# Performance work log

Measured on AMD Instinct MI355X. Metric: run time of the kernel, lower is better.

## Reference

```python
import jax, jax.numpy as jnp
import numpy as np

N, E, E_LG, H, KGE, NUM_GRAPHS, N_ITER = 100000, 500000, 1000000, 128, 128, 1024, 2
EPS = 1e-5

def _prelu(x, a):
    return jnp.where(x >= 0, x, a * x)

def _seg_mean(vals, idx, num):
    s = jax.ops.segment_sum(vals, idx, num_segments=num)
    c = jax.ops.segment_sum(jnp.ones((vals.shape[0],), vals.dtype), idx, num_segments=num)
    return s / jnp.maximum(c, 1.0)[:, None]

def setup_inputs() -> dict:
    key = jax.random.key(0)
    ks = jax.random.split(key, 16)
    sc = 1.0 / np.sqrt(H)
    inp = {
        "x": jax.random.normal(ks[0], (N, H), jnp.float32),
        "edge_attr": jax.random.normal(ks[1], (E, H), jnp.float32),
        "edge_index": jax.random.randint(ks[2], (2, E), 0, N),
        "batch": jnp.sort(jax.random.randint(ks[3], (N,), 0, NUM_GRAPHS)),
        "line_graph_edge_index": jax.random.randint(ks[4], (2, E_LG), 0, E),
        # edge_update_net: Linear + PReLU + BatchNorm1d (eval mode)
        "W1": jax.random.normal(ks[5], (H, H), jnp.float32) * sc,
        "b1": jnp.zeros((H,), jnp.float32),
        "a1": jnp.full((1,), 0.25, jnp.float32),
        "bn_gamma": jnp.ones((H,), jnp.float32),
        "bn_beta": jnp.zeros((H,), jnp.float32),
        "bn_mean": jnp.zeros((H,), jnp.float32),
        "bn_var": jnp.ones((H,), jnp.float32),
        # GRU (single layer, single step)
        "w_ih": jax.random.normal(ks[6], (3 * H, H), jnp.float32) * sc,
        "w_hh": jax.random.normal(ks[7], (3 * H, H), jnp.float32) * sc,
        "b_ih": jnp.zeros((3 * H,), jnp.float32),
        "b_hh": jnp.zeros((3 * H,), jnp.float32),
        # DynamicAttention net
        "Wa1": jax.random.normal(ks[8], (H // 2, H), jnp.float32) * sc,
        "ba1": jnp.zeros((H // 2,), jnp.float32),
        "a2": jnp.full((1,), 0.25, jnp.float32),
        "Wa2": jax.random.normal(ks[9], (1, H // 2), jnp.float32) * (1.0 / np.sqrt(H // 2)),
        "ba2": jnp.zeros((1,), jnp.float32),
        # readout
        "Wr": jax.random.normal(ks[10], (KGE, H), jnp.float32) * sc,
        "br": jnp.zeros((KGE,), jnp.float32),
    }
    return inp

def reference(x, edge_attr, W1, b1, a1, bn_gamma, bn_beta, bn_mean, bn_var,
              w_ih, w_hh, b_ih, b_hh, Wa1, ba1, a2, Wa2, ba2, Wr, br,
              edge_index, batch, line_graph_edge_index):
    src, dst = edge_index[0], edge_index[1]
    l_src, l_dst = line_graph_edge_index[0], line_graph_edge_index[1]
    h = x  # GRU hidden state [N, H]
    for _ in range(N_ITER):
        # edge-to-edge message passing (node_to_edge_proj is Identity here)
        fused = edge_attr + (x[src] + x[dst]) * 0.5  # [E, H]
        agg = _seg_mean(fused[l_src], l_dst, E)      # scatter-mean over line graph
        upd = _prelu(agg @ W1.T + b1, a1)
        upd = (upd - bn_mean) * jax.lax.rsqrt(bn_var + EPS) * bn_gamma + bn_beta
        fused = fused + upd
        node_updates = _seg_mean(fused, dst, N)      # [N, H]
        # single GRU step
        gi = node_updates @ w_ih.T + b_ih
        gh = h @ w_hh.T + b_hh
        gi_r, gi_z, gi_n = jnp.split(gi, 3, axis=-1)
        gh_r, gh_z, gh_n = jnp.split(gh, 3, axis=-1)
        r = jax.nn.sigmoid(gi_r + gh_r)
        z = jax.nn.sigmoid(gi_z + gh_z)
        n = jnp.tanh(gi_n + r * gh_n)
        h = (1.0 - z) * n + z * h
        x = h
    # dynamic attention: per-graph scalar gate
    graph_repr = _seg_mean(x, batch, NUM_GRAPHS)     # [G, H]
    attn = jax.nn.sigmoid(_prelu(graph_repr @ Wa1.T + ba1, a2) @ Wa2.T + ba2)  # [G, 1]
    attended = x * attn[batch]
    graph_emb = jax.ops.segment_sum(attended, batch, num_segments=NUM_GRAPHS)
    graph_emb = graph_emb @ Wr.T + br
    return (x, graph_emb)
```

## Files before the change

kernel.cpp:

```cpp
#include <hip/hip_runtime.h>
#include <stdint.h>

#define H 128
#define G_NUM 1024
#define BN_EPS 1e-5f
#define IDXCAP 512

typedef unsigned int uint;
typedef unsigned short ushort;
typedef unsigned char uchar;
typedef __attribute__((ext_vector_type(8))) __bf16 bf16x8;
typedef __attribute__((ext_vector_type(8))) ushort ushort8;
typedef __attribute__((ext_vector_type(4))) float f32x4;
typedef __attribute__((ext_vector_type(2))) float f32x2;

__device__ __forceinline__ float b2f(ushort u){ return __uint_as_float(((uint)u) << 16); }
__device__ __forceinline__ ushort f2b(float f){
    uint u = __float_as_uint(f);
    u += 0x7FFFu + ((u >> 16) & 1u);
    return (ushort)(u >> 16);
}
__device__ __forceinline__ float ldf(const void* p, size_t i, int bf){
    return bf ? b2f(((const ushort*)p)[i]) : ((const float*)p)[i];
}
__device__ __forceinline__ int swz(int r, int byte_in_row){
    return (r * 256 + byte_in_row) ^ ((r & 7) << 4);
}

#define GBODY(SRC, sA, sB) do{ \
    uint4 wA_ = *(const uint4*)((SRC) + (size_t)(sA) * H + ch16 * 8); \
    uint4 wB_ = *(const uint4*)((SRC) + (size_t)(sB) * H + ch16 * 8); \
    uint wa_[4] = {wA_.x, wA_.y, wA_.z, wA_.w}; \
    uint wb_[4] = {wB_.x, wB_.y, wB_.z, wB_.w}; \
    _Pragma("unroll") \
    for (int k2 = 0; k2 < 4; k2++){ \
        f32x2 va_, vb_; \
        va_.x = __uint_as_float(wa_[k2] << 16); va_.y = __uint_as_float(wa_[k2] & 0xFFFF0000u); \
        vb_.x = __uint_as_float(wb_[k2] << 16); vb_.y = __uint_as_float(wb_[k2] & 0xFFFF0000u); \
        accA[k2] += va_; accB[k2] += vb_; \
    } }while(0)

__global__ void k_setup_small(const uint* __restrict__ gamma_bits,
                              const void* b1, const void* a1, const void* gam, const void* bet,
                              const void* mean, const void* var, const void* bih, const void* bhh,
                              float* __restrict__ ep, float* __restrict__ bi, float* __restrict__ bh,
                              int* __restrict__ flag, ushort* __restrict__ fz1, ushort* __restrict__ fz2,
                              size_t zoff, int* __restrict__ off_cat, int nk_idx, int sent_val){
    __shared__ int bfs;
    int t = threadIdx.x;
    if (t == 0){
        int f = (gamma_bits[0] == 0x3F803F80u) ? 1 : 0;
        *flag = f; bfs = f;
        off_cat[nk_idx] = sent_val;
    }
    __syncthreads();
    int bf = bfs;
    bi[t] = ldf(bih, t, bf);
    bh[t] = ldf(bhh, t, bf);
    if (t < 128){
        ep[t]       = ldf(b1, t, bf);
        ep[128 + t] = rsqrtf(ldf(var, t, bf) + BN_EPS) * ldf(gam, t, bf);
        ep[256 + t] = ldf(mean, t, bf);
        ep[384 + t] = ldf(bet, t, bf);
        fz1[zoff + t] = 0; fz2[zoff + t] = 0;
    }
    if (t == 0) ep[512] = ldf(a1, 0, bf);
}

__global__ __launch_bounds__(256) void k_count2(const int* __restrict__ lgi, const int* __restrict__ ei,
                                                int* __restrict__ cnt, int ELG, int E){
    int t = blockIdx.x * 256 + threadIdx.x;
    if (t < ELG) atomicAdd(&cnt[lgi[ELG + t]], 1);
    else { int t2 = t - ELG; if (t2 < E) atomicAdd(&cnt[E + ei[E + t2]], 1); }
}
__global__ __launch_bounds__(256) void k_scan_reduce(const int* __restrict__ cnt, int* __restrict__ bsum, int n){
    int base = blockIdx.x * 1024;
    int s = 0;
    for (int i = threadIdx.x; i < 1024; i += 256){ int idx = base + i; s += (idx < n) ? cnt[idx] : 0; }
    __shared__ int r[256];
    r[threadIdx.x] = s; __syncthreads();
    for (int o = 128; o > 0; o >>= 1){ if (threadIdx.x < o) r[threadIdx.x] += r[threadIdx.x + o]; __syncthreads(); }
    if (threadIdx.x == 0) bsum[blockIdx.x] = r[0];
}
__global__ __launch_bounds__(256) void k_scan_mid(int* __restrict__ bsum, int nb){
    __shared__ int ts[256];
    int tid = threadIdx.x;
    int loc[4]; int s = 0;
    #pragma unroll
    for (int j = 0; j < 4; j++){
        int idx = tid * 4 + j;
        loc[j] = s;
        s += (idx < nb) ? bsum[idx] : 0;
    }
    ts[tid] = s; __syncthreads();
    for (int o = 1; o < 256; o <<= 1){
        int v = (tid >= o) ? ts[tid - o] : 0;
        __syncthreads();
        ts[tid] += v;
        __syncthreads();
    }
    int texcl = ts[tid] - s;
    #pragma unroll
    for (int j = 0; j < 4; j++){
        int idx = tid * 4 + j;
        if (idx < nb) bsum[idx] = texcl + loc[j];
    }
}
__global__ __launch_bounds__(256) void k_scan_final(const int* __restrict__ cnt, const int* __restrict__ bsum,
                                                    int* __restrict__ off, int n){
    __shared__ int ts[256];
    int base = blockIdx.x * 1024;
    int tid = threadIdx.x;
    int loc[4]; int s = 0;
    #pragma unroll
    for (int j = 0; j < 4; j++){
        int idx = base + tid * 4 + j;
        loc[j] = s;
        s += (idx < n) ? cnt[idx] : 0;
    }
    ts[tid] = s; __syncthreads();
    for (int o = 1; o < 256; o <<= 1){
        int v = (tid >= o) ? ts[tid - o] : 0;
        __syncthreads();
        ts[tid] += v;
        __syncthreads();
    }
    int texcl = ts[tid] - s + bsum[blockIdx.x];
    #pragma unroll
    for (int j = 0; j < 4; j++){
        int idx = base + tid * 4 + j;
        if (idx < n) off[idx] = texcl + loc[j];
    }
}
__global__ __launch_bounds__(256) void k_fill2(const int* __restrict__ lgi, const int* __restrict__ ei,
                                               const int* __restrict__ off, int* __restrict__ cur,
                                               int* __restrict__ list, int ELG, int E){
    int t = blockIdx.x * 256 + threadIdx.x;
    if (t < ELG){
        int k = lgi[ELG + t];
        int pos = atomicAdd(&cur[k], 1);
        list[off[k] + pos] = lgi[t];
    } else {
        int t2 = t - ELG;
        if (t2 < E){
            int k = E + ei[E + t2];
            int pos = atomicAdd(&cur[k], 1);
            list[off[k] + pos] = t2;
        }
    }
}
__global__ __launch_bounds__(256) void k_sortperm(const int* __restrict__ off, uchar* __restrict__ perm, int NK){
    int t = blockIdx.x * 256 + threadIdx.x;
    int wave = t >> 6;
    int l = t & 63;
    int l5 = l & 31;
    int r0 = wave * 32;
    if (r0 >= NK) return;
    int r = r0 + l5;
    int deg = off[r + 1] - off[r];
    int key = (deg << 5) | l5;
    #pragma unroll
    for (int k = 2; k <= 32; k <<= 1){
        #pragma unroll
        for (int j = k >> 1; j > 0; j >>= 1){
            int other = __shfl_xor(key, j);
            bool dir = ((l5 & k) == 0);
            bool lower = ((l5 & j) == 0);
            int mn = min(key, other), mx = max(key, other);
            key = (dir == lower) ? mn : mx;
        }
    }
    if (l < 32) perm[r0 + l5] = (uchar)(key & 31);
}
__global__ __launch_bounds__(256) void k_cvt_bf(const void* __restrict__ in, ushort* __restrict__ out,
                                                int n, const int* __restrict__ flag){
    int t = blockIdx.x * 256 + threadIdx.x;
    if (t >= n) return;
    if (*flag) out[t] = ((const ushort*)in)[t];
    else       out[t] = f2b(((const float*)in)[t]);
}
__global__ __launch_bounds__(256) void k_wcvt(const void* __restrict__ W1, const void* __restrict__ wih,
                                              const void* __restrict__ whh, const void* __restrict__ Wr,
                                              ushort* __restrict__ W1bf, ushort* __restrict__ wihbf,
                                              ushort* __restrict__ whhbf, float* __restrict__ WrT,
                                              const int* __restrict__ flag){
    int t = blockIdx.x * 256 + threadIdx.x;
    int bf = *flag;
    if (t < 16384) W1bf[t] = bf ? ((const ushort*)W1)[t] : f2b(((const float*)W1)[t]);
    else if (t < 65536){ int i = t - 16384; wihbf[i] = bf ? ((const ushort*)wih)[i] : f2b(((const float*)wih)[i]); }
    else if (t < 114688){ int i = t - 65536; whhbf[i] = bf ? ((const ushort*)whh)[i] : f2b(((const float*)whh)[i]); }
    else if (t < 131072){ int i = t - 114688; int r = i >> 7, c = i & 127; WrT[c * 128 + r] = ldf(Wr, i, bf); }
}

__global__ __launch_bounds__(256) void k_fused(const void* __restrict__ ea, const ushort* __restrict__ hb,
                                               const int* __restrict__ ei, ushort* __restrict__ fused,
                                               int E, const int* __restrict__ flag){
    int t = blockIdx.x * 256 + threadIdx.x;
    if (t >= E * 16) return;
    int bf = *flag;
    int e = t >> 4, ch = (t & 15) * 8;
    int s = ei[e], d = ei[E + e];
    ushort8 hs = *(const ushort8*)(hb + (size_t)s * H + ch);
    ushort8 hd = *(const ushort8*)(hb + (size_t)d * H + ch);
    size_t base = (size_t)e * H + ch;
    float av[8];
    if (bf){
        ushort8 a = *(const ushort8*)((const ushort*)ea + base);
        #pragma unroll
        for (int j = 0; j < 8; j++) av[j] = b2f(a[j]);
    } else {
        float4 a0 = *(const float4*)((const float*)ea + base);
        float4 a1 = *(const float4*)((const float*)ea + base + 4);
        av[0] = a0.x; av[1] = a0.y; av[2] = a0.z; av[3] = a0.w;
        av[4] = a1.x; av[5] = a1.y; av[6] = a1.z; av[7] = a1.w;
    }
    ushort8 o;
    #pragma unroll
    for (int j = 0; j < 8; j++) o[j] = f2b(av[j] + 0.5f * (b2f(hs[j]) + b2f(hd[j])));
    *(ushort8*)(fused + base) = o;
}

__global__ __launch_bounds__(256) void k_agg_gemm(const ushort* __restrict__ fused,
                                                  const int* __restrict__ off_cat, const int* __restrict__ list,
                                                  const uchar* __restrict__ perm,
                                                  const ushort* __restrict__ W1bf, const float* __restrict__ ep,
                                                  ushort* __restrict__ fused2, int E, int LMAX){
    __shared__ __attribute__((aligned(16))) char As[32 * 256];
    __shared__ int idxL[IDXCAP];
    __shared__ int offL[33];
    int tid = threadIdx.x, wid = tid >> 6, lane = tid & 63;
    int r0 = blockIdx.x * 32;
    if (tid < 33) offL[tid] = off_cat[r0 + tid];
    __syncthreads();
    int seg_s = offL[0], seglen = offL[32] - seg_s;
    bool staged = (seglen <= IDXCAP);
    if (staged){ for (int j = tid; j < seglen; j += 256) idxL[j] = list[seg_s + j]; }
    __syncthreads();
    int l16 = lane >> 4, ch16 = lane & 15;
    int rA = wid * 8 + l16, rB = rA + 4;
    int plA = perm[r0 + rA], plB = perm[r0 + rB];
    int baseA = offL[plA], degA = offL[plA + 1] - baseA;
    int baseB = offL[plB], degB = offL[plB + 1] - baseB;
    int dm = max(degA, degB);
    #pragma unroll
    for (int o = 32; o > 0; o >>= 1) dm = max(dm, __shfl_xor(dm, o));
    f32x2 accA[4] = {}, accB[4] = {};
    if (staged){
        int relA = baseA - seg_s, relB = baseB - seg_s;
        #pragma unroll 2
        for (int i = 0; i < dm; i++){
            int liA = min(relA + i, seglen - 1);
            int liB = min(relB + i, seglen - 1);
            int sA = idxL[liA];
            int sB = idxL[liB];
            sA = (i < degA) ? sA : E;
            sB = (i < degB) ? sB : E;
            GBODY(fused, sA, sB);
        }
    } else {
        #pragma unroll 2
        for (int i = 0; i < dm; i++){
            int liA = baseA + i; liA = (liA < LMAX) ? liA : (LMAX - 1);
            int liB = baseB + i; liB = (liB < LMAX) ? liB : (LMAX - 1);
            int sA = list[liA];
            int sB = list[liB];
            sA = (i < degA) ? sA : E;
            sB = (i < degB) ? sB : E;
            GBODY(fused, sA, sB);
        }
    }
    float invA = 1.f / fmaxf((float)degA, 1.f);
    float invB = 1.f / fmaxf((float)degB, 1.f);
    ushort8 oA, oB;
    #pragma unroll
    for (int k2 = 0; k2 < 4; k2++){
        oA[2 * k2] = f2b(accA[k2].x * invA); oA[2 * k2 + 1] = f2b(accA[k2].y * invA);
        oB[2 * k2] = f2b(accB[k2].x * invB); oB[2 * k2 + 1] = f2b(accB[k2].y * invB);
    }
    *(ushort8*)(As + swz(plA, ch16 * 16)) = oA;
    *(ushort8*)(As + swz(plB, ch16 * 16)) = oB;
    __syncthreads();
    int lrow = lane & 15, lhi = lane >> 4;
    f32x4 acc[2][2] = {};
    #pragma unroll
    for (int ks = 0; ks < 4; ks++){
        bf16x8 afr[2];
        #pragma unroll
        for (int rt = 0; rt < 2; rt++)
            afr[rt] = *(const bf16x8*)(As + swz(rt * 16 + lrow, ks * 64 + lhi * 16));
        #pragma unroll
        for (int cc = 0; cc < 2; cc++){
            int c = (2 * wid + cc) * 16 + lrow;
            bf16x8 bfr = *(const bf16x8*)(W1bf + (size_t)c * H + ks * 32 + lhi * 8);
            #pragma unroll
            for (int rt = 0; rt < 2; rt++)
                acc[cc][rt] = __builtin_amdgcn_mfma_f32_16x16x32_bf16(afr[rt], bfr, acc[cc][rt], 0, 0, 0);
        }
    }
    __syncthreads();
    float aa = ep[512];
    #pragma unroll
    for (int cc = 0; cc < 2; cc++){
        int c = (2 * wid + cc) * 16 + lrow;
        float bb = ep[c], sc = ep[128 + c], mb = ep[256 + c], be = ep[384 + c];
        #pragma unroll
        for (int rt = 0; rt < 2; rt++)
            #pragma unroll
            for (int rg = 0; rg < 4; rg++){
                int r = rt * 16 + lhi * 4 + rg;
                float u = acc[cc][rt][rg] + bb;
                u = (u >= 0.f) ? u : aa * u;
                u = (u - mb) * sc + be;
                *(ushort*)(As + swz(r, c * 2)) = f2b(u);
            }
    }
    __syncthreads();
    #pragma unroll
    for (int q = 0; q < 2; q++){
        int r = (q == 0) ? rA : rB;
        size_t gbase = (size_t)(r0 + r) * H + ch16 * 8;
        ushort8 f = *(const ushort8*)(fused + gbase);
        ushort8 u = *(const ushort8*)(As + swz(r, ch16 * 16));
        ushort8 o;
        #pragma unroll
        for (int j = 0; j < 8; j++) o[j] = f2b(b2f(f[j]) + b2f(u[j]));
        *(ushort8*)(fused2 + gbase) = o;
    }
}

__global__ __launch_bounds__(256) void k_gru(const ushort* __restrict__ fused2,
                                             const int* __restrict__ off_cat, const int* __restrict__ list,
                                             const uchar* __restrict__ perm,
                                             ushort* __restrict__ hb,
                                             const ushort* __restrict__ wihbf, const ushort* __restrict__ whhbf,
                                             const float* __restrict__ bi, const float* __restrict__ bh,
                                             int N, int EZ, int LMAX){
    __shared__ __attribute__((aligned(16))) char NUs[32 * 256];
    __shared__ __attribute__((aligned(16))) char HHs[32 * 256];
    __shared__ int idxL[IDXCAP];
    __shared__ int offL[33];
    int tid = threadIdx.x, wid = tid >> 6, lane = tid & 63;
    int r0 = blockIdx.x * 32;
    if (tid < 33) offL[tid] = off_cat[r0 + tid];
    int l16 = lane >> 4, ch16 = lane & 15;
    int rA = wid * 8 + l16, rB = rA + 4;
    *(ushort8*)(HHs + swz(rA, ch16 * 16)) = *(const ushort8*)(hb + (size_t)(r0 + rA) * H + ch16 * 8);
    *(ushort8*)(HHs + swz(rB, ch16 * 16)) = *(const ushort8*)(hb + (size_t)(r0 + rB) * H + ch16 * 8);
    __syncthreads();
    int seg_s = offL[0], seglen = offL[32] - seg_s;
    bool staged = (seglen <= IDXCAP);
    if (staged){ for (int j = tid; j < seglen; j += 256) idxL[j] = list[seg_s + j]; }
    __syncthreads();
    int plA = perm[r0 + rA], plB = perm[r0 + rB];
    int baseA = offL[plA], degA = offL[plA + 1] - baseA;
    int baseB = offL[plB], degB = offL[plB + 1] - baseB;
    int dm = max(degA, degB);
    #pragma unroll
    for (int o = 32; o > 0; o >>= 1) dm = max(dm, __shfl_xor(dm, o));
    f32x2 accA[4] = {}, accB[4] = {};
    if (staged){
        int relA = baseA - seg_s, relB = baseB - seg_s;
        #pragma unroll 2
        for (int i = 0; i < dm; i++){
            int liA = min(relA + i, seglen - 1);
            int liB = min(relB + i, seglen - 1);
            int sA = idxL[liA];
            int sB = idxL[liB];
            sA = (i < degA) ? sA : EZ;
            sB = (i < degB) ? sB : EZ;
            GBODY(fused2, sA, sB);
        }
    } else {
        #pragma unroll 2
        for (int i = 0; i < dm; i++){
            int liA = baseA + i; liA = (liA < LMAX) ? liA : (LMAX - 1);
            int liB = baseB + i; liB = (liB < LMAX) ? liB : (LMAX - 1);
            int sA = list[liA];
            int sB = list[liB];
            sA = (i < degA) ? sA : EZ;
            sB = (i < degB) ? sB : EZ;
            GBODY(fused2, sA, sB);
        }
    }
    float invA = 1.f / fmaxf((float)degA, 1.f);
    float invB = 1.f / fmaxf((float)degB, 1.f);
    ushort8 oA, oB;
    #pragma unroll
    for (int k2 = 0; k2 < 4; k2++){
        oA[2 * k2] = f2b(accA[k2].x * invA); oA[2 * k2 + 1] = f2b(accA[k2].y * invA);
        oB[2 * k2] = f2b(accB[k2].x * invB); oB[2 * k2 + 1] = f2b(accB[k2].y * invB);
    }
    *(ushort8*)(NUs + swz(plA, ch16 * 16)) = oA;
    *(ushort8*)(NUs + swz(plB, ch16 * 16)) = oB;
    __syncthreads();
    int lrow = lane & 15, lhi = lane >> 4;
    ushort hnew[2][2][4];
    #pragma unroll 1
    for (int b = 0; b < 2; b++){
        f32x4 aI[3][2] = {}, aH[3][2] = {};
        #pragma unroll
        for (int ks = 0; ks < 4; ks++){
            bf16x8 fN[2], fH[2];
            #pragma unroll
            for (int rt = 0; rt < 2; rt++){
                int addr = swz(rt * 16 + lrow, ks * 64 + lhi * 16);
                fN[rt] = *(const bf16x8*)(NUs + addr);
                fH[rt] = *(const bf16x8*)(HHs + addr);
            }
            #pragma unroll
            for (int g = 0; g < 3; g++){
                int c = g * 128 + (wid + 4 * b) * 16 + lrow;
                bf16x8 bI = *(const bf16x8*)(wihbf + (size_t)c * H + ks * 32 + lhi * 8);
                bf16x8 bH = *(const bf16x8*)(whhbf + (size_t)c * H + ks * 32 + lhi * 8);
                #pragma unroll
                for (int rt = 0; rt < 2; rt++){
                    aI[g][rt] = __builtin_amdgcn_mfma_f32_16x16x32_bf16(fN[rt], bI, aI[g][rt], 0, 0, 0);
                    aH[g][rt] = __builtin_amdgcn_mfma_f32_16x16x32_bf16(fH[rt], bH, aH[g][rt], 0, 0, 0);
                }
            }
        }
        int c = (wid + 4 * b) * 16 + lrow;
        float bir = bi[c], biz = bi[128 + c], bin = bi[256 + c];
        float bhr = bh[c], bhz = bh[128 + c], bhn = bh[256 + c];
        #pragma unroll
        for (int rt = 0; rt < 2; rt++)
            #pragma unroll
            for (int rg = 0; rg < 4; rg++){
                int r = rt * 16 + lhi * 4 + rg;
                float gr = aI[0][rt][rg] + bir + aH[0][rt][rg] + bhr;
                float gz = aI[1][rt][rg] + biz + aH[1][rt][rg] + bhz;
                float rv = 1.f / (1.f + __expf(-gr));
                float zv = 1.f / (1.f + __expf(-gz));
                float nv = tanhf(aI[2][rt][rg] + bin + rv * (aH[2][rt][rg] + bhn));
                float hold = b2f(*(const ushort*)(HHs + swz(r, c * 2)));
                hnew[b][rt][rg] = f2b((1.f - zv) * nv + zv * hold);
            }
    }
    __syncthreads();
    #pragma unroll
    for (int b = 0; b < 2; b++){
        int c = (wid + 4 * b) * 16 + lrow;
        #pragma unroll
        for (int rt = 0; rt < 2; rt++)
            #pragma unroll
            for (int rg = 0; rg < 4; rg++){
                int r = rt * 16 + lhi * 4 + rg;
                *(ushort*)(NUs + swz(r, c * 2)) = hnew[b][rt][rg];
            }
    }
    __syncthreads();
    *(ushort8*)(hb + (size_t)(r0 + rA) * H + ch16 * 8) = *(const ushort8*)(NUs + swz(rA, ch16 * 16));
    *(ushort8*)(hb + (size_t)(r0 + rB) * H + ch16 * 8) = *(const ushort8*)(NUs + swz(rB, ch16 * 16));
}

__global__ __launch_bounds__(256) void k_gbounds(const int* __restrict__ batch, int* __restrict__ gs, int N, int G){
    int g = blockIdx.x * 256 + threadIdx.x;
    if (g > G) return;
    int lo = 0, hi = N;
    while (lo < hi){ int mid = (lo + hi) >> 1; if (batch[mid] < g) lo = mid + 1; else hi = mid; }
    gs[g] = lo;
}
__global__ __launch_bounds__(256) void k_graph_sum(const ushort* __restrict__ hb, const int* __restrict__ gs,
                                                   float* __restrict__ gsum, void* __restrict__ out,
                                                   const int* __restrict__ flag){
    int g = blockIdx.x, c = threadIdx.x & 127, half = threadIdx.x >> 7;
    int bf = *flag;
    int s = gs[g], e = gs[g + 1];
    float acc0 = 0.f, acc1 = 0.f;
    int r = s + half;
    for (; r + 2 < e; r += 4){
        ushort u0 = hb[(size_t)r * H + c];
        ushort u1 = hb[(size_t)(r + 2) * H + c];
        float v0 = b2f(u0), v1 = b2f(u1);
        acc0 += v0; acc1 += v1;
        if (bf){ ((ushort*)out)[(size_t)r * H + c] = u0; ((ushort*)out)[(size_t)(r + 2) * H + c] = u1; }
        else   { ((float*) out)[(size_t)r * H + c] = v0; ((float*) out)[(size_t)(r + 2) * H + c] = v1; }
    }
    for (; r < e; r += 2){
        ushort u0 = hb[(size_t)r * H + c];
        float v0 = b2f(u0);
        acc0 += v0;
        if (bf) ((ushort*)out)[(size_t)r * H + c] = u0;
        else    ((float*) out)[(size_t)r * H + c] = v0;
    }
    __shared__ float tmp[128];
    if (half == 1) tmp[c] = acc0 + acc1;
    __syncthreads();
    if (half == 0) gsum[(size_t)g * H + c] = acc0 + acc1 + tmp[c];
}
__global__ void k_attn(const float* __restrict__ gsum, const int* __restrict__ gs,
                       const void* __restrict__ Wa1, const void* __restrict__ ba1,
                       const void* __restrict__ a2, const void* __restrict__ Wa2,
                       const void* __restrict__ ba2, float* __restrict__ attn, const int* __restrict__ flag){
    int g = blockIdx.x;
    int j = threadIdx.x;
    int bf = *flag;
    float inv = 1.0f / fmaxf((float)(gs[g + 1] - gs[g]), 1.0f);
    __shared__ float R[H];
    for (int i = j; i < H; i += 64) R[i] = gsum[(size_t)g * H + i] * inv;
    __syncthreads();
    float t = 0.f;
    for (int k = 0; k < H; k++) t += R[k] * ldf(Wa1, (size_t)j * H + k, bf);
    t += ldf(ba1, j, bf);
    float al = ldf(a2, 0, bf);
    t = (t >= 0.f) ? t : al * t;
    float p = t * ldf(Wa2, j, bf);
    #pragma unroll
    for (int o = 32; o > 0; o >>= 1) p += __shfl_down(p, o);
    if (j == 0) attn[g] = 1.f / (1.f + __expf(-(p + ldf(ba2, 0, bf))));
}
__global__ __launch_bounds__(256) void k_graph_gemm(const float* __restrict__ gsum, const float* __restrict__ attn,
                                                    const float* __restrict__ WrT,
                                                    const void* __restrict__ br, void* __restrict__ out,
                                                    size_t obase, const int* __restrict__ flag){
    __shared__ float A[8 * H];
    int bf = *flag;
    int r0 = blockIdx.x * 8;
    for (int i = threadIdx.x; i < 8 * H; i += 256){
        int r = i >> 7;
        A[i] = gsum[(size_t)(r0 + r) * H + (i & 127)] * attn[r0 + r];
    }
    __syncthreads();
    int c = threadIdx.x & 127;
    int rr = (threadIdx.x >> 7) * 4;
    float acc[4] = {0, 0, 0, 0};
    for (int k = 0; k < H; k++){
        float w = WrT[k * H + c];
        #pragma unroll
        for (int j = 0; j < 4; j++) acc[j] += A[(rr + j) * H + k] * w;
    }
    float bb = ldf(br, c, bf);
    for (int j = 0; j < 4; j++){
        size_t idx = obase + (size_t)(r0 + rr + j) * H + c;
        float v = acc[j] + bb;
        if (bf) ((ushort*)out)[idx] = f2b(v);
        else    ((float*) out)[idx] = v;
    }
}

extern "C" void kernel_launch(void* const* d_in, const int* in_sizes, int n_in,
                              void* d_out, int out_size, void* d_ws, size_t ws_size,
                              hipStream_t stream)
{
    const void* x    = d_in[0];
    const void* ea   = d_in[1];
    const int*  ei   = (const int*)d_in[2];
    const int*  batch= (const int*)d_in[3];
    const int*  lgi  = (const int*)d_in[4];
    const void* W1   = d_in[5];
    const void* b1   = d_in[6];
    const void* a1   = d_in[7];
    const void* bng  = d_in[8];
    const void* bnb  = d_in[9];
    const void* bnm  = d_in[10];
    const void* bnv  = d_in[11];
    const void* wih  = d_in[12];
    const void* whh  = d_in[13];
    const void* bih  = d_in[14];
    const void* bhh  = d_in[15];
    const void* Wa1  = d_in[16];
    const void* ba1  = d_in[17];
    const void* a2   = d_in[18];
    const void* Wa2  = d_in[19];
    const void* ba2  = d_in[20];
    const void* Wr   = d_in[21];
    const void* br   = d_in[22];

    const int N   = in_sizes[0] / H;
    const int E   = in_sizes[1] / H;
    const int ELG = in_sizes[4] / 2;
    const int G   = G_NUM;
    const int NK  = E + N;
    const int nb  = (NK + 1023) / 1024;

    char* ws = (char*)d_ws;
    size_t off = 0;
    auto alloc = [&](size_t b) -> void* { void* p = ws + off; off += (b + 255) & ~(size_t)255; return p; };
    int*    flag    = (int*)   alloc(256);
    ushort* hb      = (ushort*)alloc((size_t)N * H * 2);
    ushort* fused   = (ushort*)alloc((size_t)(E + 1) * H * 2);
    ushort* fused2  = (ushort*)alloc((size_t)(E + 1) * H * 2);
    int*    zreg    = (int*)   alloc((size_t)(2 * NK) * 4);
    int*    cnt_cat = zreg;
    int*    cur_cat = zreg + NK;
    int*    off_cat = (int*)   alloc((size_t)(NK + 1) * 4);
    int*    list_cat= (int*)   alloc((size_t)(ELG + E) * 4);
    uchar*  perm    = (uchar*) alloc((size_t)(NK + 32));
    int*    bsum    = (int*)   alloc((size_t)(nb + 8) * 4);
    int*    gs      = (int*)   alloc((size_t)(G + 1) * 4);
    ushort* W1bf    = (ushort*)alloc(128 * 128 * 2);
    ushort* wihbf   = (ushort*)alloc(384 * 128 * 2);
    ushort* whhbf   = (ushort*)alloc(384 * 128 * 2);
    float*  ep      = (float*) alloc(513 * 4);
    float*  bi      = (float*) alloc(384 * 4);
    float*  bh      = (float*) alloc(384 * 4);
    float*  WrT     = (float*) alloc(128 * 128 * 4);
    float*  gsum    = (float*) alloc((size_t)G * H * 4);
    float*  attn    = (float*) alloc((size_t)G * 4);

    k_setup_small<<<1, 384, 0, stream>>>((const uint*)bng, b1, a1, bng, bnb, bnm, bnv, bih, bhh,
                                         ep, bi, bh, flag, fused, fused2, (size_t)E * H,
                                         off_cat, NK, ELG + E);

    hipMemsetAsync(zreg, 0, (size_t)(2 * NK) * 4, stream);
    k_count2<<<(ELG + E + 255) / 256, 256, 0, stream>>>(lgi, ei, cnt_cat, ELG, E);
    k_scan_reduce<<<nb, 256, 0, stream>>>(cnt_cat, bsum, NK);
    k_scan_mid<<<1, 256, 0, stream>>>(bsum, nb);
    k_scan_final<<<nb, 256, 0, stream>>>(cnt_cat, bsum, off_cat, NK);
    k_fill2<<<(ELG + E + 255) / 256, 256, 0, stream>>>(lgi, ei, off_cat, cur_cat, list_cat, ELG, E);
    k_sortperm<<<(NK / 32 * 64 + 255) / 256, 256, 0, stream>>>(off_cat, perm, NK);

    k_wcvt<<<(131072 + 255) / 256, 256, 0, stream>>>(W1, wih, whh, Wr, W1bf, wihbf, whhbf, WrT, flag);

    k_cvt_bf<<<(N * H + 255) / 256, 256, 0, stream>>>(x, hb, N * H, flag);

    for (int it = 0; it < 2; it++){
        k_fused<<<(E * 16 + 255) / 256, 256, 0, stream>>>(ea, hb, ei, fused, E, flag);
        k_agg_gemm<<<(E + 31) / 32, 256, 0, stream>>>(fused, off_cat, list_cat, perm, W1bf, ep, fused2, E, ELG);
        k_gru<<<(N + 31) / 32, 256, 0, stream>>>(fused2, off_cat + E, list_cat, perm + E, hb, wihbf, whhbf, bi, bh, N, E, ELG + E);
    }

    k_gbounds<<<(G + 256) / 256, 256, 0, stream>>>(batch, gs, N, G);
    k_graph_sum<<<G, 256, 0, stream>>>(hb, gs, gsum, d_out, flag);
    k_attn<<<G, 64, 0, stream>>>(gsum, gs, Wa1, ba1, a2, Wa2, ba2, attn, flag);
    k_graph_gemm<<<G / 8, 256, 0, stream>>>(gsum, attn, WrT, br, d_out, (size_t)N * H, flag);
}
```

Before: 969.0 us.

## Renumber edges in destination-sorted order so GRU gathers read contiguous rows

Edges are relabelled by their rank in the node-destination CSR order. Edge attributes and endpoint pairs are permuted once at setup, and the line-graph CSR is built over the renumbered edges. The GRU kernel then reads contiguous fused2 rows without an index list, and the fused-edge kernel no longer converts from fp32 on each iteration. In exchange, setup gains extra kernels (rank, an extra count/scan/fill, an attribute permute) plus an E×H bf16 buffer, and the line-graph gather in the aggregation kernel stays random.

```diff
diff --git a/kernel.cpp b/kernel.cpp
--- a/kernel.cpp
+++ b/kernel.cpp
@@ -45,13 +45,15 @@
                               const void* mean, const void* var, const void* bih, const void* bhh,
                               float* __restrict__ ep, float* __restrict__ bi, float* __restrict__ bh,
                               int* __restrict__ flag, ushort* __restrict__ fz1, ushort* __restrict__ fz2,
-                              size_t zoff, int* __restrict__ off_cat, int nk_idx, int sent_val){
+                              size_t zoff, int* __restrict__ lg_off, int E, int ELG,
+                              int* __restrict__ nd_off, int N, int Etot){
     __shared__ int bfs;
     int t = threadIdx.x;
     if (t == 0){
         int f = (gamma_bits[0] == 0x3F803F80u) ? 1 : 0;
         *flag = f; bfs = f;
-        off_cat[nk_idx] = sent_val;
+        lg_off[E] = ELG;
+        nd_off[N] = Etot;
     }
     __syncthreads();
     int bf = bfs;
@@ -67,11 +69,39 @@
     if (t == 0) ep[512] = ldf(a1, 0, bf);
 }
 
-__global__ __launch_bounds__(256) void k_count2(const int* __restrict__ lgi, const int* __restrict__ ei,
-                                                int* __restrict__ cnt, int ELG, int E){
-    int t = blockIdx.x * 256 + threadIdx.x;
-    if (t < ELG) atomicAdd(&cnt[lgi[ELG + t]], 1);
-    else { int t2 = t - ELG; if (t2 < E) atomicAdd(&cnt[E + ei[E + t2]], 1); }
+__global__ __launch_bounds__(256) void k_count_nd(const int* __restrict__ ei, int* __restrict__ cnt, int E){
+    int t = blockIdx.x * 256 + threadIdx.x;
+    if (t < E) atomicAdd(&cnt[ei[E + t]], 1);
+}
+__global__ __launch_bounds__(256) void k_fill_nd(const int* __restrict__ ei, const int* __restrict__ off,
+                                                 int* __restrict__ cur, int* __restrict__ list, int E){
+    int t = blockIdx.x * 256 + threadIdx.x;
+    if (t >= E) return;
+    int k = ei[E + t];
+    int pos = atomicAdd(&cur[k], 1);
+    list[off[k] + pos] = t;
+}
+__global__ __launch_bounds__(256) void k_rank(const int* __restrict__ nd_list, int* __restrict__ rank,
+                                              int2* __restrict__ eis, const int* __restrict__ ei, int E){
+    int j = blockIdx.x * 256 + threadIdx.x;
+    if (j >= E) return;
+    int e = nd_list[j];
+    rank[e] = j;
+    eis[j] = make_int2(ei[e], ei[E + e]);
+}
+__global__ __launch_bounds__(256) void k_count_lg(const int* __restrict__ lgi, const int* __restrict__ rank,
+                                                  int* __restrict__ cnt, int ELG){
+    int t = blockIdx.x * 256 + threadIdx.x;
+    if (t < ELG) atomicAdd(&cnt[rank[lgi[ELG + t]]], 1);
+}
+__global__ __launch_bounds__(256) void k_fill_lg(const int* __restrict__ lgi, const int* __restrict__ rank,
+                                                 const int* __restrict__ off, int* __restrict__ cur,
+                                                 int* __restrict__ list, int ELG){
+    int t = blockIdx.x * 256 + threadIdx.x;
+    if (t >= ELG) return;
+    int k = rank[lgi[ELG + t]];
+    int pos = atomicAdd(&cur[k], 1);
+    list[off[k] + pos] = rank[lgi[t]];
 }
 __global__ __launch_bounds__(256) void k_scan_reduce(const int* __restrict__ cnt, int* __restrict__ bsum, int n){
     int base = blockIdx.x * 1024;
@@ -132,23 +162,6 @@
         if (idx < n) off[idx] = texcl + loc[j];
     }
 }
-__global__ __launch_bounds__(256) void k_fill2(const int* __restrict__ lgi, const int* __restrict__ ei,
-                                               const int* __restrict__ off, int* __restrict__ cur,
-                                               int* __restrict__ list, int ELG, int E){
-    int t = blockIdx.x * 256 + threadIdx.x;
-    if (t < ELG){
-        int k = lgi[ELG + t];
-        int pos = atomicAdd(&cur[k], 1);
-        list[off[k] + pos] = lgi[t];
-    } else {
-        int t2 = t - ELG;
-        if (t2 < E){
-            int k = E + ei[E + t2];
-            int pos = atomicAdd(&cur[k], 1);
-            list[off[k] + pos] = t2;
-        }
-    }
-}
 __global__ __launch_bounds__(256) void k_sortperm(const int* __restrict__ off, uchar* __restrict__ perm, int NK){
     int t = blockIdx.x * 256 + threadIdx.x;
     int wave = t >> 6;
@@ -172,6 +185,25 @@
     }
     if (l < 32) perm[r0 + l5] = (uchar)(key & 31);
 }
+__global__ __launch_bounds__(256) void k_eaperm(const void* __restrict__ ea, const int* __restrict__ nd_list,
+                                                ushort* __restrict__ ea_s, int E, const int* __restrict__ flag){
+    int t = blockIdx.x * 256 + threadIdx.x;
+    if (t >= E * 16) return;
+    int bf = *flag;
+    int j = t >> 4, ch = (t & 15) * 8;
+    int e = nd_list[j];
+    size_t src = (size_t)e * H + ch;
+    ushort8 o;
+    if (bf){
+        o = *(const ushort8*)((const ushort*)ea + src);
+    } else {
+        float4 a0 = *(const float4*)((const float*)ea + src);
+        float4 a1 = *(const float4*)((const float*)ea + src + 4);
+        o[0] = f2b(a0.x); o[1] = f2b(a0.y); o[2] = f2b(a0.z); o[3] = f2b(a0.w);
+        o[4] = f2b(a1.x); o[5] = f2b(a1.y); o[6] = f2b(a1.z); o[7] = f2b(a1.w);
+    }
+    *(ushort8*)(ea_s + (size_t)j * H + ch) = o;
+}
 __global__ __launch_bounds__(256) void k_cvt_bf(const void* __restrict__ in, ushort* __restrict__ out,
                                                 int n, const int* __restrict__ flag){
     int t = blockIdx.x * 256 + threadIdx.x;
@@ -192,36 +224,24 @@
     else if (t < 131072){ int i = t - 114688; int r = i >> 7, c = i & 127; WrT[c * 128 + r] = ldf(Wr, i, bf); }
 }
 
-__global__ __launch_bounds__(256) void k_fused(const void* __restrict__ ea, const ushort* __restrict__ hb,
-                                               const int* __restrict__ ei, ushort* __restrict__ fused,
-                                               int E, const int* __restrict__ flag){
+__global__ __launch_bounds__(256) void k_fused(const ushort* __restrict__ ea_s, const ushort* __restrict__ hb,
+                                               const int2* __restrict__ eis, ushort* __restrict__ fused, int E){
     int t = blockIdx.x * 256 + threadIdx.x;
     if (t >= E * 16) return;
-    int bf = *flag;
-    int e = t >> 4, ch = (t & 15) * 8;
-    int s = ei[e], d = ei[E + e];
-    ushort8 hs = *(const ushort8*)(hb + (size_t)s * H + ch);
-    ushort8 hd = *(const ushort8*)(hb + (size_t)d * H + ch);
-    size_t base = (size_t)e * H + ch;
-    float av[8];
-    if (bf){
-        ushort8 a = *(const ushort8*)((const ushort*)ea + base);
-        #pragma unroll
-        for (int j = 0; j < 8; j++) av[j] = b2f(a[j]);
-    } else {
-        float4 a0 = *(const float4*)((const float*)ea + base);
-        float4 a1 = *(const float4*)((const float*)ea + base + 4);
-        av[0] = a0.x; av[1] = a0.y; av[2] = a0.z; av[3] = a0.w;
-        av[4] = a1.x; av[5] = a1.y; av[6] = a1.z; av[7] = a1.w;
-    }
+    int j = t >> 4, ch = (t & 15) * 8;
+    int2 sd = eis[j];
+    size_t base = (size_t)j * H + ch;
+    ushort8 hs = *(const ushort8*)(hb + (size_t)sd.x * H + ch);
+    ushort8 hd = *(const ushort8*)(hb + (size_t)sd.y * H + ch);
+    ushort8 a = *(const ushort8*)(ea_s + base);
     ushort8 o;
     #pragma unroll
-    for (int j = 0; j < 8; j++) o[j] = f2b(av[j] + 0.5f * (b2f(hs[j]) + b2f(hd[j])));
+    for (int k = 0; k < 8; k++) o[k] = f2b(b2f(a[k]) + 0.5f * (b2f(hs[k]) + b2f(hd[k])));
     *(ushort8*)(fused + base) = o;
 }
 
 __global__ __launch_bounds__(256) void k_agg_gemm(const ushort* __restrict__ fused,
-                                                  const int* __restrict__ off_cat, const int* __restrict__ list,
+                                                  const int* __restrict__ lg_off, const int* __restrict__ list,
                                                   const uchar* __restrict__ perm,
                                                   const ushort* __restrict__ W1bf, const float* __restrict__ ep,
                                                   ushort* __restrict__ fused2, int E, int LMAX){
@@ -230,7 +250,7 @@
     __shared__ int offL[33];
     int tid = threadIdx.x, wid = tid >> 6, lane = tid & 63;
     int r0 = blockIdx.x * 32;
-    if (tid < 33) offL[tid] = off_cat[r0 + tid];
+    if (tid < 33) offL[tid] = lg_off[r0 + tid];
     __syncthreads();
     int seg_s = offL[0], seglen = offL[32] - seg_s;
     bool staged = (seglen <= IDXCAP);
@@ -329,28 +349,23 @@
 }
 
 __global__ __launch_bounds__(256) void k_gru(const ushort* __restrict__ fused2,
-                                             const int* __restrict__ off_cat, const int* __restrict__ list,
+                                             const int* __restrict__ nd_off,
                                              const uchar* __restrict__ perm,
                                              ushort* __restrict__ hb,
                                              const ushort* __restrict__ wihbf, const ushort* __restrict__ whhbf,
                                              const float* __restrict__ bi, const float* __restrict__ bh,
-                                             int N, int EZ, int LMAX){
+                                             int N, int EZ){
     __shared__ __attribute__((aligned(16))) char NUs[32 * 256];
     __shared__ __attribute__((aligned(16))) char HHs[32 * 256];
-    __shared__ int idxL[IDXCAP];
     __shared__ int offL[33];
     int tid = threadIdx.x, wid = tid >> 6, lane = tid & 63;
     int r0 = blockIdx.x * 32;
-    if (tid < 33) offL[tid] = off_cat[r0 + tid];
+    if (tid < 33) offL[tid] = nd_off[r0 + tid];
     int l16 = lane >> 4, ch16 = lane & 15;
     int rA = wid * 8 + l16, rB = rA + 4;
     *(ushort8*)(HHs + swz(rA, ch16 * 16)) = *(const ushort8*)(hb + (size_t)(r0 + rA) * H + ch16 * 8);
     *(ushort8*)(HHs + swz(rB, ch16 * 16)) = *(const ushort8*)(hb + (size_t)(r0 + rB) * H + ch16 * 8);
     __syncthreads();
-    int seg_s = offL[0], seglen = offL[32] - seg_s;
-    bool staged = (seglen <= IDXCAP);
-    if (staged){ for (int j = tid; j < seglen; j += 256) idxL[j] = list[seg_s + j]; }
-    __syncthreads();
     int plA = perm[r0 + rA], plB = perm[r0 + rB];
     int baseA = offL[plA], degA = offL[plA + 1] - baseA;
     int baseB = offL[plB], degB = offL[plB + 1] - baseB;
@@ -358,29 +373,11 @@
     #pragma unroll
     for (int o = 32; o > 0; o >>= 1) dm = max(dm, __shfl_xor(dm, o));
     f32x2 accA[4] = {}, accB[4] = {};
-    if (staged){
-        int relA = baseA - seg_s, relB = baseB - seg_s;
-        #pragma unroll 2
-        for (int i = 0; i < dm; i++){
-            int liA = min(relA + i, seglen - 1);
-            int liB = min(relB + i, seglen - 1);
-            int sA = idxL[liA];
-            int sB = idxL[liB];
-            sA = (i < degA) ? sA : EZ;
-            sB = (i < degB) ? sB : EZ;
-            GBODY(fused2, sA, sB);
-        }
-    } else {
-        #pragma unroll 2
-        for (int i = 0; i < dm; i++){
-            int liA = baseA + i; liA = (liA < LMAX) ? liA : (LMAX - 1);
-            int liB = baseB + i; liB = (liB < LMAX) ? liB : (LMAX - 1);
-            int sA = list[liA];
-            int sB = list[liB];
-            sA = (i < degA) ? sA : EZ;
-            sB = (i < degB) ? sB : EZ;
-            GBODY(fused2, sA, sB);
-        }
+    #pragma unroll 2
+    for (int i = 0; i < dm; i++){
+        int sA = (i < degA) ? (baseA + i) : EZ;
+        int sB = (i < degB) ? (baseB + i) : EZ;
+        GBODY(fused2, sA, sB);
     }
     float invA = 1.f / fmaxf((float)degA, 1.f);
     float invB = 1.f / fmaxf((float)degB, 1.f);
@@ -570,23 +567,32 @@
     const int E   = in_sizes[1] / H;
     const int ELG = in_sizes[4] / 2;
     const int G   = G_NUM;
-    const int NK  = E + N;
-    const int nb  = (NK + 1023) / 1024;
+    const int nb_lg = (E + 1023) / 1024;
+    const int nb_nd = (N + 1023) / 1024;
 
     char* ws = (char*)d_ws;
     size_t off = 0;
     auto alloc = [&](size_t b) -> void* { void* p = ws + off; off += (b + 255) & ~(size_t)255; return p; };
     int*    flag    = (int*)   alloc(256);
     ushort* hb      = (ushort*)alloc((size_t)N * H * 2);
+    ushort* ea_s    = (ushort*)alloc((size_t)E * H * 2);
     ushort* fused   = (ushort*)alloc((size_t)(E + 1) * H * 2);
     ushort* fused2  = (ushort*)alloc((size_t)(E + 1) * H * 2);
-    int*    zreg    = (int*)   alloc((size_t)(2 * NK) * 4);
-    int*    cnt_cat = zreg;
-    int*    cur_cat = zreg + NK;
-    int*    off_cat = (int*)   alloc((size_t)(NK + 1) * 4);
-    int*    list_cat= (int*)   alloc((size_t)(ELG + E) * 4);
-    uchar*  perm    = (uchar*) alloc((size_t)(NK + 32));
-    int*    bsum    = (int*)   alloc((size_t)(nb + 8) * 4);
+    int*    zreg    = (int*)   alloc((size_t)(2 * E + 2 * N) * 4);
+    int*    lg_cnt  = zreg;
+    int*    lg_cur  = zreg + E;
+    int*    nd_cnt  = zreg + 2 * E;
+    int*    nd_cur  = zreg + 2 * E + N;
+    int*    lg_off  = (int*)   alloc((size_t)(E + 1) * 4);
+    int*    nd_off  = (int*)   alloc((size_t)(N + 1) * 4);
+    int*    lg_list = (int*)   alloc((size_t)ELG * 4);
+    int*    nd_list = (int*)   alloc((size_t)E * 4);
+    int*    rank    = (int*)   alloc((size_t)E * 4);
+    int2*   eis     = (int2*)  alloc((size_t)E * 8);
+    uchar*  perm_lg = (uchar*) alloc((size_t)(E + 32));
+    uchar*  perm_nd = (uchar*) alloc((size_t)(N + 32));
+    int*    bsumA   = (int*)   alloc((size_t)(nb_lg + 8) * 4);
+    int*    bsumB   = (int*)   alloc((size_t)(nb_nd + 8) * 4);
     int*    gs      = (int*)   alloc((size_t)(G + 1) * 4);
     ushort* W1bf    = (ushort*)alloc(128 * 128 * 2);
     ushort* wihbf   = (ushort*)alloc(384 * 128 * 2);
@@ -600,24 +606,32 @@
 
     k_setup_small<<<1, 384, 0, stream>>>((const uint*)bng, b1, a1, bng, bnb, bnm, bnv, bih, bhh,
                                          ep, bi, bh, flag, fused, fused2, (size_t)E * H,
-                                         off_cat, NK, ELG + E);
-
-    hipMemsetAsync(zreg, 0, (size_t)(2 * NK) * 4, stream);
-    k_count2<<<(ELG + E + 255) / 256, 256, 0, stream>>>(lgi, ei, cnt_cat, ELG, E);
-    k_scan_reduce<<<nb, 256, 0, stream>>>(cnt_cat, bsum, NK);
-    k_scan_mid<<<1, 256, 0, stream>>>(bsum, nb);
-    k_scan_final<<<nb, 256, 0, stream>>>(cnt_cat, bsum, off_cat, NK);
-    k_fill2<<<(ELG + E + 255) / 256, 256, 0, stream>>>(lgi, ei, off_cat, cur_cat, list_cat, ELG, E);
-    k_sortperm<<<(NK / 32 * 64 + 255) / 256, 256, 0, stream>>>(off_cat, perm, NK);
+                                         lg_off, E, ELG, nd_off, N, E);
+
+    hipMemsetAsync(zreg, 0, (size_t)(2 * E + 2 * N) * 4, stream);
+    k_count_nd<<<(E + 255) / 256, 256, 0, stream>>>(ei, nd_cnt, E);
+    k_scan_reduce<<<nb_nd, 256, 0, stream>>>(nd_cnt, bsumB, N);
+    k_scan_mid<<<1, 256, 0, stream>>>(bsumB, nb_nd);
+    k_scan_final<<<nb_nd, 256, 0, stream>>>(nd_cnt, bsumB, nd_off, N);
+    k_fill_nd<<<(E + 255) / 256, 256, 0, stream>>>(ei, nd_off, nd_cur, nd_list, E);
+    k_rank<<<(E + 255) / 256, 256, 0, stream>>>(nd_list, rank, eis, ei, E);
+    k_count_lg<<<(ELG + 255) / 256, 256, 0, stream>>>(lgi, rank, lg_cnt, ELG);
+    k_scan_reduce<<<nb_lg, 256, 0, stream>>>(lg_cnt, bsumA, E);
+    k_scan_mid<<<1, 256, 0, stream>>>(bsumA, nb_lg);
+    k_scan_final<<<nb_lg, 256, 0, stream>>>(lg_cnt, bsumA, lg_off, E);
+    k_fill_lg<<<(ELG + 255) / 256, 256, 0, stream>>>(lgi, rank, lg_off, lg_cur, lg_list, ELG);
+    k_sortperm<<<(E / 32 * 64 + 255) / 256, 256, 0, stream>>>(lg_off, perm_lg, E);
+    k_sortperm<<<(N / 32 * 64 + 255) / 256, 256, 0, stream>>>(nd_off, perm_nd, N);
+    k_eaperm<<<(E * 16 + 255) / 256, 256, 0, stream>>>(ea, nd_list, ea_s, E, flag);
 
     k_wcvt<<<(131072 + 255) / 256, 256, 0, stream>>>(W1, wih, whh, Wr, W1bf, wihbf, whhbf, WrT, flag);
 
     k_cvt_bf<<<(N * H + 255) / 256, 256, 0, stream>>>(x, hb, N * H, flag);
 
     for (int it = 0; it < 2; it++){
-        k_fused<<<(E * 16 + 255) / 256, 256, 0, stream>>>(ea, hb, ei, fused, E, flag);
-        k_agg_gemm<<<(E + 31) / 32, 256, 0, stream>>>(fused, off_cat, list_cat, perm, W1bf, ep, fused2, E, ELG);
-        k_gru<<<(N + 31) / 32, 256, 0, stream>>>(fused2, off_cat + E, list_cat, perm + E, hb, wihbf, whhbf, bi, bh, N, E, ELG + E);
+        k_fused<<<(E * 16 + 255) / 256, 256, 0, stream>>>(ea_s, hb, eis, fused, E);
+        k_agg_gemm<<<(E + 31) / 32, 256, 0, stream>>>(fused, lg_off, lg_list, perm_lg, W1bf, ep, fused2, E, ELG);
+        k_gru<<<(N + 31) / 32, 256, 0, stream>>>(fused2, nd_off, perm_nd, hb, wihbf, whhbf, bi, bh, N, E);
     }
 
     k_gbounds<<<(G + 256) / 256, 256, 0, stream>>>(batch, gs, N, G);
```

New measurement: 1.012 ms. +4.4%, slower.
